# Kernel optimization log

Measured on AMD Instinct MI355X. Metric: run time of the kernel, lower is better.

## Reference

```python
import jax, jax.numpy as jnp
import numpy as np

B, L, DIM = 16, 131072, 9  # batch, audio samples, 1 fundamental + 8 harmonics
SR = 22050.0
SINE_AMP = 0.1
NOISE_STD = 0.003


def setup_inputs() -> dict:
    key = jax.random.key(0)
    k1, k2, k3, k4 = jax.random.split(key, 4)
    u = jax.random.uniform(k1, (B, L, 1), dtype=jnp.float32)
    voiced = jax.random.uniform(k2, (B, L, 1), dtype=jnp.float32) > 0.3
    f0 = jnp.where(voiced, 100.0 + 300.0 * u, 0.0)  # Hz, 0 where unvoiced
    rand_ini = jax.random.uniform(k3, (B, DIM), dtype=jnp.float32)
    rand_ini = rand_ini.at[:, 0].set(0.0)  # first harmonic gets no random phase
    noise_z = jax.random.normal(k4, (B, L, DIM), dtype=jnp.float32)
    return {"f0": f0, "rand_ini": rand_ini, "noise_z": noise_z}


def reference(f0, rand_ini, noise_z):
    dim = noise_z.shape[-1]
    two_pi = 2.0 * jnp.pi
    # harmonic multiples of f0: (B, L, dim)
    k = jnp.arange(1, dim + 1, dtype=f0.dtype)
    fn = f0 * k
    # normalized per-step phase increment in [0, 1)
    rad = jnp.mod(fn / SR, 1.0)
    rad = rad.at[:, 0, :].add(rand_ini)  # random initial phase per harmonic
    # wrap-around detection: cumulative phase mod 1 decreases at a wrap
    tmp_over_one = jnp.mod(jnp.cumsum(rad, axis=1), 1.0)
    wrap = (tmp_over_one[:, 1:, :] - tmp_over_one[:, :-1, :]) < 0.0
    cumsum_shift = jnp.concatenate(
        [jnp.zeros_like(rad[:, :1, :]), jnp.where(wrap, -1.0, 0.0).astype(rad.dtype)],
        axis=1,
    )
    sines = jnp.sin(jnp.cumsum(rad + cumsum_shift, axis=1) * two_pi)
    sine_waves = sines * SINE_AMP
    # voiced/unvoiced mask from fundamental f0
    uv = (f0 > 0.0).astype(f0.dtype)  # (B, L, 1)
    noise_amp = uv * NOISE_STD + (1.0 - uv) * (SINE_AMP / 3.0)
    noise = noise_amp * noise_z
    sine_waves = sine_waves * uv + noise
    return sine_waves, uv, noise
```

## Files before the change

### kernel.cpp

```cpp
#include <hip/hip_runtime.h>
#include <math.h>


#define Bq 16
#define Lq 131072
#define DIMq 9
#define CHUNK 1024
#define NCHUNK (Lq / CHUNK)
#define NBLK (Bq * NCHUNK)
#define NT 256
#define PT 4
#define Q4 (CHUNK * DIMq / 4 / NT)

typedef float f32x4 __attribute__((ext_vector_type(4)));
typedef double f64x2 __attribute__((ext_vector_type(2)));

__global__ void __launch_bounds__(NT, 8) k_partials(
    const float* __restrict__ f0, double* __restrict__ part) {
  int bc = blockIdx.x;
  int b = bc >> 7, c = bc & 127;
  int tid = threadIdx.x, lane = tid & 63, wave = tid >> 6;
  const f32x4* p = (const f32x4*)(f0 + (size_t)b * Lq + (size_t)c * CHUNK);
  f32x4 x = p[tid];
  double s = ((double)x.x + (double)x.y) + ((double)x.z + (double)x.w);
#pragma unroll
  for (int d = 32; d > 0; d >>= 1) s += __shfl_xor(s, d, 64);
  __shared__ double ws[NT / 64];
  if (lane == 0) ws[wave] = s;
  __syncthreads();
  if (tid == 0) part[bc] = (ws[0] + ws[1]) + (ws[2] + ws[3]);
}

__global__ void __launch_bounds__(NT, 8) k_main(
    const float* __restrict__ f0, const float* __restrict__ rini,
    const float* __restrict__ nz, const double* __restrict__ part,
    float* __restrict__ out0, float* __restrict__ out1,
    float* __restrict__ out2) {
  int bc = blockIdx.x;
  int b = bc >> 7, c = bc & 127;
  int tid = threadIdx.x, lane = tid & 63, wave = tid >> 6;
  size_t t0g = (size_t)b * Lq + (size_t)c * CHUNK;

  __shared__ float p1s[CHUNK + CHUNK / 8];
  __shared__ float nmps[CHUNK + CHUNK / 8];
  __shared__ float inis[DIMq];
  __shared__ double wsum[NT / 64];

  f32x4 fa = *(const f32x4*)(f0 + t0g + tid * PT);
  float fv[PT] = {fa.x, fa.y, fa.z, fa.w};
  double run = 0.0, inc[PT];
#pragma unroll
  for (int j = 0; j < PT; ++j) { run += (double)fv[j]; inc[j] = run; }
  double tot = run;
#pragma unroll
  for (int d = 1; d < 64; d <<= 1) {
    double o = __shfl_up(tot, d, 64);
    if (lane >= d) tot += o;
  }
  if (lane == 63) wsum[wave] = tot;
  if (tid < DIMq) inis[tid] = rini[b * DIMq + tid];
  __syncthreads();

  f64x2 pp = ((const f64x2*)(part + (b << 7)))[lane];
  double pv = ((2 * lane < c) ? pp.x : 0.0) + ((2 * lane + 1 < c) ? pp.y : 0.0);
#pragma unroll
  for (int d = 32; d > 0; d >>= 1) pv += __shfl_xor(pv, d, 64);
  double wpre = 0.0;
  for (int w = 0; w < wave; ++w) wpre += wsum[w];
  double base = pv + wpre + (tot - run);

  const double invsr = 1.0 / 22050.0;
  const float nampU = (float)(0.1 / 3.0);
  float uvv[PT];
#pragma unroll
  for (int j = 0; j < PT; ++j) {
    double ph = (base + inc[j]) * invsr;
    ph -= floor(ph);
    int t = tid * PT + j;
    p1s[t + (t >> 3)] = (float)ph;
    bool v = fv[j] > 0.0f;
    nmps[t + (t >> 3)] = v ? 0.003f : -nampU;
    uvv[j] = v ? 1.0f : 0.0f;
  }
  f32x4 u0 = {uvv[0], uvv[1], uvv[2], uvv[3]};
  __builtin_nontemporal_store(u0, (f32x4*)(out1 + t0g + tid * PT));
  __syncthreads();

  const f32x4* nzc = (const f32x4*)(nz + t0g * DIMq);
  f32x4* o0c = (f32x4*)(out0 + t0g * DIMq);
  f32x4* o2c = (f32x4*)(out2 + t0g * DIMq);

  struct R { float r0, r2; };
  auto gen = [&](int t, int d, float nzv) -> R {
    int ti = t + (t >> 3);
    float p1 = p1s[ti], nm = nmps[ti];
    float ph = (float)(d + 1) * p1 + inis[d];
    ph -= floorf(ph);
    float s = __builtin_amdgcn_sinf(ph) * 0.1f;
    float noise = fabsf(nm) * nzv;
    R r;
    r.r2 = noise;
    r.r0 = (nm > 0.0f) ? s + noise : noise;
    return r;
  };

#pragma unroll 3
  for (int w = 0; w < Q4; ++w) {
    int q = w * NT + tid;
    int e = q * 4;
    int t = (int)(((unsigned)e * 7282u) >> 16);
    int d = e - t * 9;
    f32x4 nzv = nzc[q];
    R a = gen(t, d, nzv.x); if (++d == 9) { d = 0; ++t; }
    R bb = gen(t, d, nzv.y); if (++d == 9) { d = 0; ++t; }
    R cc = gen(t, d, nzv.z); if (++d == 9) { d = 0; ++t; }
    R dd = gen(t, d, nzv.w);
    f32x4 r0 = {a.r0, bb.r0, cc.r0, dd.r0};
    f32x4 r2 = {a.r2, bb.r2, cc.r2, dd.r2};
    __builtin_nontemporal_store(r0, &o0c[q]);
    __builtin_nontemporal_store(r2, &o2c[q]);
  }
}

extern "C" void kernel_launch(void* const* d_in, const int* in_sizes, int n_in,
                              void* d_out, int out_size, void* d_ws, size_t ws_size,
                              hipStream_t stream) {
  const float* f0 = (const float*)d_in[0];
  const float* rini = (const float*)d_in[1];
  const float* nz = (const float*)d_in[2];
  float* out = (float*)d_out;
  float* out0 = out;
  float* out1 = out + (size_t)Bq * Lq * DIMq;
  float* out2 = out1 + (size_t)Bq * Lq;
  double* part = (double*)d_ws;

  k_partials<<<NBLK, NT, 0, stream>>>(f0, part);
  k_main<<<NBLK, NT, 0, stream>>>(f0, rini, nz, part, out0, out1, out2);
}
```

Baseline: 46.02 us.

## Keep per-thread timesteps in registers instead of LDS for harmonic generation

Each thread now handles its own 4 timesteps × 9 harmonics (36 contiguous floats) straight from registers. This removes the LDS staging of phase and noise-amplitude, the second barrier, and the runtime t/d index math. The per-thread chunk is fully unrolled, and nontemporal stores are replaced with plain stores. In exchange, accesses are no longer coalesced across lanes: each lane strides by 144 bytes per vector load or store. The occupancy hint is also lowered from 8 to 4 blocks per CU to allow more registers.

Result: slower. 104.9 us (+127.9%).

```diff
diff --git a/kernel.cpp b/kernel.cpp
--- a/kernel.cpp
+++ b/kernel.cpp
@@ -10,7 +10,7 @@
 #define NBLK (Bq * NCHUNK)
 #define NT 256
 #define PT 4
-#define Q4 (CHUNK * DIMq / 4 / NT)
+#define TQ 9
 
 typedef float f32x4 __attribute__((ext_vector_type(4)));
 typedef double f64x2 __attribute__((ext_vector_type(2)));
@@ -31,7 +31,7 @@
   if (tid == 0) part[bc] = (ws[0] + ws[1]) + (ws[2] + ws[3]);
 }
 
-__global__ void __launch_bounds__(NT, 8) k_main(
+__global__ void __launch_bounds__(NT, 4) k_main(
     const float* __restrict__ f0, const float* __restrict__ rini,
     const float* __restrict__ nz, const double* __restrict__ part,
     float* __restrict__ out0, float* __restrict__ out1,
@@ -41,9 +41,6 @@
   int tid = threadIdx.x, lane = tid & 63, wave = tid >> 6;
   size_t t0g = (size_t)b * Lq + (size_t)c * CHUNK;
 
-  __shared__ float p1s[CHUNK + CHUNK / 8];
-  __shared__ float nmps[CHUNK + CHUNK / 8];
-  __shared__ float inis[DIMq];
   __shared__ double wsum[NT / 64];
 
   f32x4 fa = *(const f32x4*)(f0 + t0g + tid * PT);
@@ -58,7 +55,6 @@
     if (lane >= d) tot += o;
   }
   if (lane == 63) wsum[wave] = tot;
-  if (tid < DIMq) inis[tid] = rini[b * DIMq + tid];
   __syncthreads();
 
   f64x2 pp = ((const f64x2*)(part + (b << 7)))[lane];
@@ -71,54 +67,46 @@
 
   const double invsr = 1.0 / 22050.0;
   const float nampU = (float)(0.1 / 3.0);
-  float uvv[PT];
+  float p1r[PT], nmr[PT], uvv[PT];
 #pragma unroll
   for (int j = 0; j < PT; ++j) {
     double ph = (base + inc[j]) * invsr;
     ph -= floor(ph);
-    int t = tid * PT + j;
-    p1s[t + (t >> 3)] = (float)ph;
+    p1r[j] = (float)ph;
     bool v = fv[j] > 0.0f;
-    nmps[t + (t >> 3)] = v ? 0.003f : -nampU;
+    nmr[j] = v ? 0.003f : -nampU;
     uvv[j] = v ? 1.0f : 0.0f;
   }
   f32x4 u0 = {uvv[0], uvv[1], uvv[2], uvv[3]};
-  __builtin_nontemporal_store(u0, (f32x4*)(out1 + t0g + tid * PT));
-  __syncthreads();
+  *(f32x4*)(out1 + t0g + tid * PT) = u0;
 
-  const f32x4* nzc = (const f32x4*)(nz + t0g * DIMq);
-  f32x4* o0c = (f32x4*)(out0 + t0g * DIMq);
-  f32x4* o2c = (f32x4*)(out2 + t0g * DIMq);
+  float inir[DIMq];
+#pragma unroll
+  for (int d = 0; d < DIMq; ++d) inir[d] = rini[b * DIMq + d];
 
-  struct R { float r0, r2; };
-  auto gen = [&](int t, int d, float nzv) -> R {
-    int ti = t + (t >> 3);
-    float p1 = p1s[ti], nm = nmps[ti];
-    float ph = (float)(d + 1) * p1 + inis[d];
-    ph -= floorf(ph);
-    float s = __builtin_amdgcn_sinf(ph) * 0.1f;
-    float noise = fabsf(nm) * nzv;
-    R r;
-    r.r2 = noise;
-    r.r0 = (nm > 0.0f) ? s + noise : noise;
-    return r;
-  };
+  const f32x4* nzp = (const f32x4*)(nz + (t0g + (size_t)tid * PT) * DIMq);
+  f32x4* o0p = (f32x4*)(out0 + (t0g + (size_t)tid * PT) * DIMq);
+  f32x4* o2p = (f32x4*)(out2 + (t0g + (size_t)tid * PT) * DIMq);
 
-#pragma unroll 3
-  for (int w = 0; w < Q4; ++w) {
-    int q = w * NT + tid;
-    int e = q * 4;
-    int t = (int)(((unsigned)e * 7282u) >> 16);
-    int d = e - t * 9;
-    f32x4 nzv = nzc[q];
-    R a = gen(t, d, nzv.x); if (++d == 9) { d = 0; ++t; }
-    R bb = gen(t, d, nzv.y); if (++d == 9) { d = 0; ++t; }
-    R cc = gen(t, d, nzv.z); if (++d == 9) { d = 0; ++t; }
-    R dd = gen(t, d, nzv.w);
-    f32x4 r0 = {a.r0, bb.r0, cc.r0, dd.r0};
-    f32x4 r2 = {a.r2, bb.r2, cc.r2, dd.r2};
-    __builtin_nontemporal_store(r0, &o0c[q]);
-    __builtin_nontemporal_store(r2, &o2c[q]);
+#pragma unroll
+  for (int q = 0; q < TQ; ++q) {
+    f32x4 nzv = nzp[q];
+    f32x4 r0, r2;
+#pragma unroll
+    for (int comp = 0; comp < 4; ++comp) {
+      const int e = q * 4 + comp;
+      const int tl = e / 9;
+      const int d = e - tl * 9;
+      float p1 = p1r[tl], nm = nmr[tl];
+      float ph = (float)(d + 1) * p1 + inir[d];
+      ph -= floorf(ph);
+      float s = __builtin_amdgcn_sinf(ph) * 0.1f;
+      float noise = fabsf(nm) * nzv[comp];
+      r2[comp] = noise;
+      r0[comp] = (nm > 0.0f) ? s + noise : noise;
+    }
+    o0p[q] = r0;
+    o2p[q] = r2;
   }
 }
 
```

## Double main-kernel tile to 2048 samples with 512 threads and pack LDS pairs

Applied to the files above, without the earlier changes.

The main kernel now handles 2048-sample tiles with 512 threads, which halves the block count. Each lane sums two partial chunks, so the prefix offset is built from pairs. The phase and noise-amplitude arrays in shared memory are merged into one interleaved float2 array, so each element needs one LDS read instead of two. The per-harmonic random phases go into registers instead of shared memory, and floor-subtract is replaced with hardware fract. The larger blocks may reduce occupancy and lengthen the serial scan, and the fp32 fract near 1.0 could differ slightly from the old floor-based wrap.

Measured after the change: 47.13 us. 1.02x slower.

```diff
diff --git a/kernel.cpp b/kernel.cpp
--- a/kernel.cpp
+++ b/kernel.cpp
@@ -7,12 +7,16 @@
 #define DIMq 9
 #define CHUNK 1024
 #define NCHUNK (Lq / CHUNK)
-#define NBLK (Bq * NCHUNK)
+#define NPBLK (Bq * NCHUNK)
+#define BT 2048
+#define NMBLK (Bq * (Lq / BT))
 #define NT 256
+#define NT2 512
 #define PT 4
-#define Q4 (CHUNK * DIMq / 4 / NT)
+#define Q4 (BT * DIMq / 4 / NT2)
 
 typedef float f32x4 __attribute__((ext_vector_type(4)));
+typedef float f32x2 __attribute__((ext_vector_type(2)));
 typedef double f64x2 __attribute__((ext_vector_type(2)));
 
 __global__ void __launch_bounds__(NT, 8) k_partials(
@@ -31,20 +35,18 @@
   if (tid == 0) part[bc] = (ws[0] + ws[1]) + (ws[2] + ws[3]);
 }
 
-__global__ void __launch_bounds__(NT, 8) k_main(
+__global__ void __launch_bounds__(NT2, 8) k_main(
     const float* __restrict__ f0, const float* __restrict__ rini,
     const float* __restrict__ nz, const double* __restrict__ part,
     float* __restrict__ out0, float* __restrict__ out1,
     float* __restrict__ out2) {
   int bc = blockIdx.x;
-  int b = bc >> 7, c = bc & 127;
+  int b = bc >> 6, cp = bc & 63;
   int tid = threadIdx.x, lane = tid & 63, wave = tid >> 6;
-  size_t t0g = (size_t)b * Lq + (size_t)c * CHUNK;
+  size_t t0g = (size_t)b * Lq + (size_t)cp * BT;
 
-  __shared__ float p1s[CHUNK + CHUNK / 8];
-  __shared__ float nmps[CHUNK + CHUNK / 8];
-  __shared__ float inis[DIMq];
-  __shared__ double wsum[NT / 64];
+  __shared__ f32x2 ps[BT];
+  __shared__ double wsum[NT2 / 64];
 
   f32x4 fa = *(const f32x4*)(f0 + t0g + tid * PT);
   float fv[PT] = {fa.x, fa.y, fa.z, fa.w};
@@ -58,11 +60,10 @@
     if (lane >= d) tot += o;
   }
   if (lane == 63) wsum[wave] = tot;
-  if (tid < DIMq) inis[tid] = rini[b * DIMq + tid];
   __syncthreads();
 
   f64x2 pp = ((const f64x2*)(part + (b << 7)))[lane];
-  double pv = ((2 * lane < c) ? pp.x : 0.0) + ((2 * lane + 1 < c) ? pp.y : 0.0);
+  double pv = (lane < cp) ? (pp.x + pp.y) : 0.0;
 #pragma unroll
   for (int d = 32; d > 0; d >>= 1) pv += __shfl_xor(pv, d, 64);
   double wpre = 0.0;
@@ -74,16 +75,18 @@
   float uvv[PT];
 #pragma unroll
   for (int j = 0; j < PT; ++j) {
-    double ph = (base + inc[j]) * invsr;
-    ph -= floor(ph);
-    int t = tid * PT + j;
-    p1s[t + (t >> 3)] = (float)ph;
+    double ph = __builtin_amdgcn_fract((base + inc[j]) * invsr);
     bool v = fv[j] > 0.0f;
-    nmps[t + (t >> 3)] = v ? 0.003f : -nampU;
+    f32x2 e = {(float)ph, v ? 0.003f : -nampU};
+    ps[tid * PT + j] = e;
     uvv[j] = v ? 1.0f : 0.0f;
   }
   f32x4 u0 = {uvv[0], uvv[1], uvv[2], uvv[3]};
   __builtin_nontemporal_store(u0, (f32x4*)(out1 + t0g + tid * PT));
+
+  float inir[DIMq];
+#pragma unroll
+  for (int d = 0; d < DIMq; ++d) inir[d] = rini[b * DIMq + d];
   __syncthreads();
 
   const f32x4* nzc = (const f32x4*)(nz + t0g * DIMq);
@@ -92,21 +95,19 @@
 
   struct R { float r0, r2; };
   auto gen = [&](int t, int d, float nzv) -> R {
-    int ti = t + (t >> 3);
-    float p1 = p1s[ti], nm = nmps[ti];
-    float ph = (float)(d + 1) * p1 + inis[d];
-    ph -= floorf(ph);
+    f32x2 e = ps[t];
+    float ph = __builtin_amdgcn_fractf((float)(d + 1) * e.x + inir[d]);
     float s = __builtin_amdgcn_sinf(ph) * 0.1f;
-    float noise = fabsf(nm) * nzv;
+    float noise = fabsf(e.y) * nzv;
     R r;
     r.r2 = noise;
-    r.r0 = (nm > 0.0f) ? s + noise : noise;
+    r.r0 = (e.y > 0.0f) ? s + noise : noise;
     return r;
   };
 
 #pragma unroll 3
   for (int w = 0; w < Q4; ++w) {
-    int q = w * NT + tid;
+    int q = w * NT2 + tid;
     int e = q * 4;
     int t = (int)(((unsigned)e * 7282u) >> 16);
     int d = e - t * 9;
@@ -134,6 +135,6 @@
   float* out2 = out1 + (size_t)Bq * Lq;
   double* part = (double*)d_ws;
 
-  k_partials<<<NBLK, NT, 0, stream>>>(f0, part);
-  k_main<<<NBLK, NT, 0, stream>>>(f0, rini, nz, part, out0, out1, out2);
+  k_partials<<<NPBLK, NT, 0, stream>>>(f0, part);
+  k_main<<<NMBLK, NT2, 0, stream>>>(f0, rini, nz, part, out0, out1, out2);
 }
```
